# Optimization experiments

Hardware: AMD Instinct MI355X
Metric: run time of the kernel (lower is better)

Reference implementation:

```python
import jax, jax.numpy as jnp
import numpy as np

EPS = 1e-8  # torch F.cosine_similarity default eps


def setup_inputs() -> dict:
    key = jax.random.key(0)
    k1, k2 = jax.random.split(key)
    B, D, C = 8192, 1024, 1000
    x = jax.random.normal(k1, (B, D), dtype=jnp.float32)
    W = jax.random.normal(k2, (D, C), dtype=jnp.float32) * 0.02
    b = jnp.zeros((C,), dtype=jnp.float32)
    return {"x": x, "W": W, "b": b}


def reference(x, W, b):
    B = x.shape[0]
    # classifier logits -> softmax probs
    logits = x @ W + b                              # [B, C]
    logp = jax.nn.log_softmax(logits, axis=1)       # [B, C]
    pred = jnp.exp(logp)
    # per-row sum of p * log p (negative entropy), matches pred*log(pred) loop
    loss = jnp.sum(pred * logp, axis=-1)            # [B]
    # per-row mean cosine similarity against all rows (incl. self)
    norms = jnp.maximum(jnp.linalg.norm(x, axis=1, keepdims=True), EPS)
    xn = x / norms                                  # [B, D]
    sim = xn @ xn.T                                 # [B, B]
    weight = jnp.sum(sim, axis=1) / B               # [B]
    return loss * weight
```

## Files before the change

kernel.cpp:

```cpp
#include <hip/hip_runtime.h>
#include <hip/hip_bf16.h>
#include <cstdint>
#include <cstddef>

typedef __attribute__((ext_vector_type(8))) short bf16x8;
typedef __attribute__((ext_vector_type(4))) float f32x4;

__device__ __forceinline__ unsigned short f2bf(float f) {
  union { float f; unsigned u; } v; v.f = f;
  unsigned r = v.u + 0x7FFFu + ((v.u >> 16) & 1u);
  return (unsigned short)(r >> 16);
}

__device__ __forceinline__ float bf2f(unsigned short h) {
  union { float f; unsigned u; } c; c.u = ((unsigned)h) << 16;
  return c.f;
}

__device__ __forceinline__ void gload_lds16(const void* g, void* l) {
  __builtin_amdgcn_global_load_lds(
      (const __attribute__((address_space(1))) unsigned int*)g,
      (__attribute__((address_space(3))) unsigned int*)l, 16, 0, 0);
}

__global__ __launch_bounds__(1024) void k01_prep(const float* __restrict__ W,
                                                 unsigned short* __restrict__ Wt,
                                                 const float* __restrict__ x,
                                                 unsigned short* __restrict__ xbf,
                                                 float* __restrict__ rnorm,
                                                 float* __restrict__ s) {
  __shared__ __align__(16) char sm[82176];
  int tid = threadIdx.x;
  int b = blockIdx.x;
  int lane = tid & 63;
  int wid = tid >> 6;

  int k0 = (b & 15) * 64;
  int c0 = (b >> 4) * 64;
  int tx = tid & 63;
  int ty = tid >> 6;
  float wreg[4];
#pragma unroll
  for (int i = 0; i < 4; ++i) {
    int c = c0 + tx;
    wreg[i] = (c < 1000) ? W[(size_t)(k0 + i * 16 + ty) * 1000 + c] : 0.f;
  }

  {
    float (*sblk)[1024] = (float(*)[1024])sm;
    int row0 = b * 32 + wid * 2;
    const float4* xr0 = (const float4*)(x + (size_t)row0 * 1024);
    const float4* xr1 = (const float4*)(x + (size_t)(row0 + 1) * 1024);
    float4 v[2][4];
#pragma unroll
    for (int j = 0; j < 4; ++j) v[0][j] = xr0[lane + j * 64];
#pragma unroll
    for (int j = 0; j < 4; ++j) v[1][j] = xr1[lane + j * 64];
    float ss0 = 0.f, ss1 = 0.f;
#pragma unroll
    for (int j = 0; j < 4; ++j) {
      ss0 += v[0][j].x * v[0][j].x + v[0][j].y * v[0][j].y +
             v[0][j].z * v[0][j].z + v[0][j].w * v[0][j].w;
      ss1 += v[1][j].x * v[1][j].x + v[1][j].y * v[1][j].y +
             v[1][j].z * v[1][j].z + v[1][j].w * v[1][j].w;
    }
#pragma unroll
    for (int m = 1; m < 64; m <<= 1) {
      ss0 += __shfl_xor(ss0, m);
      ss1 += __shfl_xor(ss1, m);
    }
    float rn0 = 1.f / fmaxf(sqrtf(ss0), 1e-8f);
    float rn1 = 1.f / fmaxf(sqrtf(ss1), 1e-8f);
    if (lane == 0) {
      rnorm[row0] = rn0;
      rnorm[row0 + 1] = rn1;
    }
    float4 sacc[4];
#pragma unroll
    for (int j = 0; j < 4; ++j) {
      ushort4 h0, h1;
      h0.x = f2bf(v[0][j].x); h0.y = f2bf(v[0][j].y);
      h0.z = f2bf(v[0][j].z); h0.w = f2bf(v[0][j].w);
      h1.x = f2bf(v[1][j].x); h1.y = f2bf(v[1][j].y);
      h1.z = f2bf(v[1][j].z); h1.w = f2bf(v[1][j].w);
      ((ushort4*)(xbf + (size_t)row0 * 1024))[lane + j * 64] = h0;
      ((ushort4*)(xbf + (size_t)(row0 + 1) * 1024))[lane + j * 64] = h1;
      sacc[j].x = v[0][j].x * rn0 + v[1][j].x * rn1;
      sacc[j].y = v[0][j].y * rn0 + v[1][j].y * rn1;
      sacc[j].z = v[0][j].z * rn0 + v[1][j].z * rn1;
      sacc[j].w = v[0][j].w * rn0 + v[1][j].w * rn1;
    }
#pragma unroll
    for (int j = 0; j < 4; ++j) ((float4*)sblk[wid])[j * 64 + lane] = sacc[j];
    __syncthreads();
    float t = 0.f;
#pragma unroll
    for (int w = 0; w < 16; ++w) t += sblk[w][tid];
    atomicAdd(&s[tid], t);
  }

  {
    float (*tile)[65] = (float(*)[65])(sm + 65536);
#pragma unroll
    for (int i = 0; i < 4; ++i) tile[i * 16 + ty][tx] = wreg[i];
    __syncthreads();
#pragma unroll
    for (int i = 0; i < 4; ++i) {
      int ct = i * 16 + ty;
      Wt[(size_t)(c0 + ct) * 1024 + (k0 + tx)] = f2bf(tile[tx][ct]);
    }
  }
}

#define LDSBUF 49152

__global__ __launch_bounds__(512) void k3_gemm(const unsigned short* __restrict__ xbf,
                                               const unsigned short* __restrict__ wt,
                                               const float* __restrict__ bias,
                                               float* __restrict__ pm,
                                               float* __restrict__ pz,
                                               float* __restrict__ ps) {
  __shared__ __align__(16) char lds[147456];

  int tid = threadIdx.x;
  int lane = tid & 63;
  int wid = tid >> 6;
  int wc = wid & 1;
  int wr = wid >> 1;
  int cb = blockIdx.x >> 5;
  int rb = blockIdx.x & 31;
  int C0 = cb * 128;
  int R0 = rb * 256;

  float bv[4][4];
#pragma unroll
  for (int mf = 0; mf < 4; ++mf)
#pragma unroll
    for (int q = 0; q < 4; ++q) {
      int cls_g = C0 + wc * 64 + mf * 16 + (lane >> 4) * 4 + q;
      bv[mf][q] = (cls_g < 1000) ? bias[cls_g] : -1e30f;
    }
  f32x4 acc[4][4];
#pragma unroll
  for (int mf = 0; mf < 4; ++mf)
#pragma unroll
    for (int nf = 0; nf < 4; ++nf)
#pragma unroll
      for (int q = 0; q < 4; ++q) acc[mf][nf][q] = bv[mf][q];

  const char* gA = (const char*)(wt + (size_t)C0 * 1024);
  const char* gB = (const char*)(xbf + (size_t)R0 * 1024);
  int grow = lane >> 3;
  int gswz = ((lane & 7) ^ grow) << 4;

#define STA(kt, b, r)                                                          \
  gload_lds16(gA + (size_t)((r) * 64 + wid * 8 + grow) * 2048 + (kt) * 128 +   \
                  gswz,                                                        \
              lds + (b) * LDSBUF + (r) * 8192 + wid * 1024)
#define STB(kt, b, r)                                                          \
  gload_lds16(gB + (size_t)((r) * 64 + wid * 8 + grow) * 2048 + (kt) * 128 +   \
                  gswz,                                                        \
              lds + (b) * LDSBUF + 16384 + (r) * 8192 + wid * 1024)

  STA(0, 0, 0); STA(0, 0, 1); STB(0, 0, 0); STB(0, 0, 1); STB(0, 0, 2); STB(0, 0, 3);
  STA(1, 1, 0); STA(1, 1, 1); STB(1, 1, 0); STB(1, 1, 1); STB(1, 1, 2); STB(1, 1, 3);

  int rsw = (lane & 7) << 4;
  int kcol = (lane >> 4) * 16;

  auto ktile = [&](const char* A, const char* B, int nt, int nb, bool pf) {
    bf16x8 a[4][2];
#pragma unroll
    for (int mf = 0; mf < 4; ++mf)
#pragma unroll
      for (int ks = 0; ks < 2; ++ks)
        a[mf][ks] = *(const bf16x8*)(A + (wc * 64 + mf * 16 + (lane & 15)) * 128 +
                                     ((ks * 64 + kcol) ^ rsw));
    {
      bf16x8 b0[2];
#pragma unroll
      for (int ks = 0; ks < 2; ++ks)
        b0[ks] = *(const bf16x8*)(B + (wr * 64 + 0 * 16 + (lane & 15)) * 128 +
                                  ((ks * 64 + kcol) ^ rsw));
      if (pf) { STA(nt, nb, 0); STA(nt, nb, 1); }
      __builtin_amdgcn_s_barrier();
      __builtin_amdgcn_s_setprio(1);
#pragma unroll
      for (int ks = 0; ks < 2; ++ks)
#pragma unroll
        for (int mf = 0; mf < 4; ++mf)
          acc[mf][0] = __builtin_amdgcn_mfma_f32_16x16x32_bf16(a[mf][ks], b0[ks],
                                                               acc[mf][0], 0, 0, 0);
      __builtin_amdgcn_s_setprio(0);
      __builtin_amdgcn_s_barrier();
    }
    {
      bf16x8 b1[2];
#pragma unroll
      for (int ks = 0; ks < 2; ++ks)
        b1[ks] = *(const bf16x8*)(B + (wr * 64 + 1 * 16 + (lane & 15)) * 128 +
                                  ((ks * 64 + kcol) ^ rsw));
      if (pf) { STB(nt, nb, 0); STB(nt, nb, 1); }
      __builtin_amdgcn_s_barrier();
      __builtin_amdgcn_s_setprio(1);
#pragma unroll
      for (int ks = 0; ks < 2; ++ks)
#pragma unroll
        for (int mf = 0; mf < 4; ++mf)
          acc[mf][1] = __builtin_amdgcn_mfma_f32_16x16x32_bf16(a[mf][ks], b1[ks],
                                                               acc[mf][1], 0, 0, 0);
      __builtin_amdgcn_s_setprio(0);
      __builtin_amdgcn_s_barrier();
    }
    {
      bf16x8 b2[2];
#pragma unroll
      for (int ks = 0; ks < 2; ++ks)
        b2[ks] = *(const bf16x8*)(B + (wr * 64 + 2 * 16 + (lane & 15)) * 128 +
                                  ((ks * 64 + kcol) ^ rsw));
      if (pf) { STB(nt, nb, 2); STB(nt, nb, 3); }
      __builtin_amdgcn_s_barrier();
      __builtin_amdgcn_s_setprio(1);
#pragma unroll
      for (int ks = 0; ks < 2; ++ks)
#pragma unroll
        for (int mf = 0; mf < 4; ++mf)
          acc[mf][2] = __builtin_amdgcn_mfma_f32_16x16x32_bf16(a[mf][ks], b2[ks],
                                                               acc[mf][2], 0, 0, 0);
      __builtin_amdgcn_s_setprio(0);
      __builtin_amdgcn_s_barrier();
    }
    {
      bf16x8 b3[2];
#pragma unroll
      for (int ks = 0; ks < 2; ++ks)
        b3[ks] = *(const bf16x8*)(B + (wr * 64 + 3 * 16 + (lane & 15)) * 128 +
                                  ((ks * 64 + kcol) ^ rsw));
      __builtin_amdgcn_s_barrier();
      __builtin_amdgcn_s_setprio(1);
#pragma unroll
      for (int ks = 0; ks < 2; ++ks)
#pragma unroll
        for (int mf = 0; mf < 4; ++mf)
          acc[mf][3] = __builtin_amdgcn_mfma_f32_16x16x32_bf16(a[mf][ks], b3[ks],
                                                               acc[mf][3], 0, 0, 0);
      __builtin_amdgcn_s_setprio(0);
    }
  };

  for (int t = 0; t < 15; ++t) {
    asm volatile("s_waitcnt vmcnt(6)" ::: "memory");
    __builtin_amdgcn_s_barrier();
    asm volatile("" ::: "memory");
    const char* A = lds + (t % 3) * LDSBUF;
    ktile(A, A + 16384, t + 2, (t + 2) % 3, t < 14);
  }
  asm volatile("s_waitcnt vmcnt(0)" ::: "memory");
  __builtin_amdgcn_s_barrier();
  asm volatile("" ::: "memory");
  {
    const char* A = lds + (15 % 3) * LDSBUF;
    ktile(A, A + 16384, 0, 0, false);
  }

  __syncthreads();
  float* mm = (float*)lds;
  float* zz = mm + 512;
  float* sv = zz + 512;
#pragma unroll
  for (int nf = 0; nf < 4; ++nf) {
    float m1 = -1e30f;
#pragma unroll
    for (int mf = 0; mf < 4; ++mf)
#pragma unroll
      for (int q = 0; q < 4; ++q) m1 = fmaxf(m1, acc[mf][nf][q]);
    m1 = fmaxf(m1, __shfl_xor(m1, 16));
    m1 = fmaxf(m1, __shfl_xor(m1, 32));
    float z1 = 0.f, s1 = 0.f;
#pragma unroll
    for (int mf = 0; mf < 4; ++mf)
#pragma unroll
      for (int q = 0; q < 4; ++q) {
        float tt = acc[mf][nf][q] - m1;
        float e = expf(tt);
        z1 += e;
        s1 += e * tt;
      }
    z1 += __shfl_xor(z1, 16); z1 += __shfl_xor(z1, 32);
    s1 += __shfl_xor(s1, 16); s1 += __shfl_xor(s1, 32);
    if (lane < 16) {
      int r = wr * 64 + nf * 16 + lane;
      mm[wc * 256 + r] = m1;
      zz[wc * 256 + r] = z1;
      sv[wc * 256 + r] = s1;
    }
  }
  __syncthreads();
  if (tid < 256) {
    float m0 = mm[tid], mA = mm[256 + tid];
    float z0 = zz[tid], zA = zz[256 + tid];
    float s0 = sv[tid], sA = sv[256 + tid];
    float M = fmaxf(m0, mA);
    float e0 = expf(m0 - M), e1 = expf(mA - M);
    float Z = z0 * e0 + zA * e1;
    float S = e0 * (s0 + (m0 - M) * z0) + e1 * (sA + (mA - M) * zA);
    size_t o = (size_t)cb * 8192 + R0 + tid;
    pm[o] = M;
    pz[o] = Z;
    ps[o] = S;
  }
}

__global__ __launch_bounds__(256) void k4_final(const unsigned short* __restrict__ xbf,
                                                const float* __restrict__ s,
                                                const float* __restrict__ rnorm,
                                                const float* __restrict__ pm,
                                                const float* __restrict__ pz,
                                                const float* __restrict__ ps,
                                                float* __restrict__ out) {
  int tid = threadIdx.x;
  int wid = tid >> 6, lane = tid & 63;
  int row = blockIdx.x * 4 + wid;
  const bf16x8* xr = (const bf16x8*)(xbf + (size_t)row * 1024);
  const float4* s4 = (const float4*)s;
  float dot = 0.f;
#pragma unroll
  for (int j = 0; j < 2; ++j) {
    bf16x8 v = xr[lane + j * 64];
    float4 sa = s4[(lane + j * 64) * 2];
    float4 sb = s4[(lane + j * 64) * 2 + 1];
    dot += bf2f((unsigned short)v[0]) * sa.x + bf2f((unsigned short)v[1]) * sa.y +
           bf2f((unsigned short)v[2]) * sa.z + bf2f((unsigned short)v[3]) * sa.w +
           bf2f((unsigned short)v[4]) * sb.x + bf2f((unsigned short)v[5]) * sb.y +
           bf2f((unsigned short)v[6]) * sb.z + bf2f((unsigned short)v[7]) * sb.w;
  }
#pragma unroll
  for (int m = 1; m < 64; m <<= 1) dot += __shfl_xor(dot, m);
  if (lane == 0) {
    float mv[8], zv[8], svv[8];
    float M = -1e30f;
#pragma unroll
    for (int c = 0; c < 8; ++c) {
      mv[c] = pm[(size_t)c * 8192 + row];
      zv[c] = pz[(size_t)c * 8192 + row];
      svv[c] = ps[(size_t)c * 8192 + row];
      M = fmaxf(M, mv[c]);
    }
    float Z = 0.f, S = 0.f;
#pragma unroll
    for (int c = 0; c < 8; ++c) {
      float e = expf(mv[c] - M);
      Z += zv[c] * e;
      S += e * (svv[c] + (mv[c] - M) * zv[c]);
    }
    float loss = S / Z - logf(Z);
    out[row] = loss * dot * rnorm[row] * (1.f / 8192.f);
  }
}

extern "C" void kernel_launch(void* const* d_in, const int* in_sizes, int n_in,
                              void* d_out, int out_size, void* d_ws, size_t ws_size,
                              hipStream_t stream) {
  (void)in_sizes; (void)n_in; (void)out_size; (void)ws_size;
  const float* x = (const float*)d_in[0];
  const float* W = (const float*)d_in[1];
  const float* b = (const float*)d_in[2];
  float* out = (float*)d_out;
  char* ws = (char*)d_ws;

  unsigned short* Wt = (unsigned short*)(ws + 0);
  unsigned short* xbf = (unsigned short*)(ws + 2097152);
  float* rnorm = (float*)(ws + 18874368);
  float* s = (float*)(ws + 18907136);
  float* pm = (float*)(ws + 18915328);
  float* pz = (float*)(ws + 18915328 + 262144);
  float* ps = (float*)(ws + 18915328 + 524288);

  hipMemsetAsync(s, 0, 4096, stream);
  k01_prep<<<256, 1024, 0, stream>>>(W, Wt, x, xbf, rnorm, s);
  k3_gemm<<<256, 512, 0, stream>>>(xbf, Wt, b, pm, pz, ps);
  k4_final<<<2048, 256, 0, stream>>>(xbf, s, rnorm, pm, pz, ps, out);
}
```

Measured before the change: 52.22 us.

## Replace atomic column-sum with partial buffer reduction and simplify GEMM tiling

The prep kernel now writes per-block partial column sums to a buffer, and a new small reduction kernel sums them, replacing the memset plus atomicAdd path. The GEMM kernel moves from 512-thread blocks with 256-row tiles and a 3-stage, finely barriered pipeline to 256-thread blocks with 128-row tiles, a simple double buffer and one sync per k-step, launching twice as many blocks with less LDS each. This aims to remove atomic contention and raise occupancy, at the cost of an extra kernel launch and less overlap between loads and MFMA. The sp buffer aliases pm, which is safe only because the reduction kernel finishes before the GEMM writes pm.

```diff
diff --git a/kernel.cpp b/kernel.cpp
--- a/kernel.cpp
+++ b/kernel.cpp
@@ -28,7 +28,7 @@
                                                  const float* __restrict__ x,
                                                  unsigned short* __restrict__ xbf,
                                                  float* __restrict__ rnorm,
-                                                 float* __restrict__ s) {
+                                                 float* __restrict__ sp) {
   __shared__ __align__(16) char sm[82176];
   int tid = threadIdx.x;
   int b = blockIdx.x;
@@ -93,10 +93,10 @@
 #pragma unroll
     for (int j = 0; j < 4; ++j) ((float4*)sblk[wid])[j * 64 + lane] = sacc[j];
     __syncthreads();
-    float t = 0.f;
-#pragma unroll
-    for (int w = 0; w < 16; ++w) t += sblk[w][tid];
-    atomicAdd(&s[tid], t);
+    float acc = 0.f;
+#pragma unroll
+    for (int w = 0; w < 16; ++w) acc += sblk[w][tid];
+    sp[(size_t)b * 1024 + tid] = acc;
   }
 
   {
@@ -112,25 +112,38 @@
   }
 }
 
-#define LDSBUF 49152
-
-__global__ __launch_bounds__(512) void k3_gemm(const unsigned short* __restrict__ xbf,
+__global__ __launch_bounds__(256) void k2_sred(const float* __restrict__ sp,
+                                               float* __restrict__ s) {
+  __shared__ float red[4][64];
+  int t = threadIdx.x;
+  int dd = t & 63;
+  int g = t >> 6;
+  int d = blockIdx.x * 64 + dd;
+  float acc = 0.f;
+#pragma unroll 8
+  for (int b = g * 64; b < g * 64 + 64; ++b) acc += sp[(size_t)b * 1024 + d];
+  red[g][dd] = acc;
+  __syncthreads();
+  if (g == 0) s[d] = red[0][dd] + red[1][dd] + red[2][dd] + red[3][dd];
+}
+
+__global__ __launch_bounds__(256) void k3_gemm(const unsigned short* __restrict__ xbf,
                                                const unsigned short* __restrict__ wt,
                                                const float* __restrict__ bias,
                                                float* __restrict__ pm,
                                                float* __restrict__ pz,
                                                float* __restrict__ ps) {
-  __shared__ __align__(16) char lds[147456];
+  __shared__ __align__(16) char lds[65536];
 
   int tid = threadIdx.x;
   int lane = tid & 63;
   int wid = tid >> 6;
   int wc = wid & 1;
   int wr = wid >> 1;
-  int cb = blockIdx.x >> 5;
-  int rb = blockIdx.x & 31;
+  int cb = blockIdx.x >> 6;
+  int rb = blockIdx.x & 63;
   int C0 = cb * 128;
-  int R0 = rb * 256;
+  int R0 = rb * 128;
 
   float bv[4][4];
 #pragma unroll
@@ -150,123 +163,64 @@
 
   const char* gA = (const char*)(wt + (size_t)C0 * 1024);
   const char* gB = (const char*)(xbf + (size_t)R0 * 1024);
-  int grow = lane >> 3;
-  int gswz = ((lane & 7) ^ grow) << 4;
-
-#define STA(kt, b, r)                                                          \
-  gload_lds16(gA + (size_t)((r) * 64 + wid * 8 + grow) * 2048 + (kt) * 128 +   \
-                  gswz,                                                        \
-              lds + (b) * LDSBUF + (r) * 8192 + wid * 1024)
-#define STB(kt, b, r)                                                          \
-  gload_lds16(gB + (size_t)((r) * 64 + wid * 8 + grow) * 2048 + (kt) * 128 +   \
-                  gswz,                                                        \
-              lds + (b) * LDSBUF + 16384 + (r) * 8192 + wid * 1024)
-
-  STA(0, 0, 0); STA(0, 0, 1); STB(0, 0, 0); STB(0, 0, 1); STB(0, 0, 2); STB(0, 0, 3);
-  STA(1, 1, 0); STA(1, 1, 1); STB(1, 1, 0); STB(1, 1, 1); STB(1, 1, 2); STB(1, 1, 3);
+  int grow = (tid >> 3) & 7;
+  int gswz = ((tid & 7) ^ grow) << 4;
+
+  auto stage = [&](int kt, int bb) {
+    char* lA = lds + bb * 32768;
+    char* lB = lA + 16384;
+#pragma unroll
+    for (int i = 0; i < 4; ++i) {
+      size_t row = i * 32 + (tid >> 3);
+      gload_lds16(gA + row * 2048 + kt * 128 + gswz, lA + i * 4096 + tid * 16);
+    }
+#pragma unroll
+    for (int i = 0; i < 4; ++i) {
+      size_t row = i * 32 + (tid >> 3);
+      gload_lds16(gB + row * 2048 + kt * 128 + gswz, lB + i * 4096 + tid * 16);
+    }
+  };
 
   int rsw = (lane & 7) << 4;
   int kcol = (lane >> 4) * 16;
 
-  auto ktile = [&](const char* A, const char* B, int nt, int nb, bool pf) {
-    bf16x8 a[4][2];
+  stage(0, 0);
+  __syncthreads();
+  int cur = 0;
+  for (int t = 0; t < 16; ++t) {
+    if (t < 15) stage(t + 1, cur ^ 1);
+    const char* A = lds + cur * 32768;
+    const char* B = A + 16384;
+    bf16x8 a[4][2], bb[4][2];
 #pragma unroll
     for (int mf = 0; mf < 4; ++mf)
 #pragma unroll
       for (int ks = 0; ks < 2; ++ks)
         a[mf][ks] = *(const bf16x8*)(A + (wc * 64 + mf * 16 + (lane & 15)) * 128 +
                                      ((ks * 64 + kcol) ^ rsw));
-    {
-      bf16x8 b0[2];
+#pragma unroll
+    for (int nf = 0; nf < 4; ++nf)
 #pragma unroll
       for (int ks = 0; ks < 2; ++ks)
-        b0[ks] = *(const bf16x8*)(B + (wr * 64 + 0 * 16 + (lane & 15)) * 128 +
-                                  ((ks * 64 + kcol) ^ rsw));
-      if (pf) { STA(nt, nb, 0); STA(nt, nb, 1); }
-      __builtin_amdgcn_s_barrier();
-      __builtin_amdgcn_s_setprio(1);
-#pragma unroll
-      for (int ks = 0; ks < 2; ++ks)
-#pragma unroll
-        for (int mf = 0; mf < 4; ++mf)
-          acc[mf][0] = __builtin_amdgcn_mfma_f32_16x16x32_bf16(a[mf][ks], b0[ks],
-                                                               acc[mf][0], 0, 0, 0);
-      __builtin_amdgcn_s_setprio(0);
-      __builtin_amdgcn_s_barrier();
-    }
-    {
-      bf16x8 b1[2];
-#pragma unroll
-      for (int ks = 0; ks < 2; ++ks)
-        b1[ks] = *(const bf16x8*)(B + (wr * 64 + 1 * 16 + (lane & 15)) * 128 +
-                                  ((ks * 64 + kcol) ^ rsw));
-      if (pf) { STB(nt, nb, 0); STB(nt, nb, 1); }
-      __builtin_amdgcn_s_barrier();
-      __builtin_amdgcn_s_setprio(1);
-#pragma unroll
-      for (int ks = 0; ks < 2; ++ks)
-#pragma unroll
-        for (int mf = 0; mf < 4; ++mf)
-          acc[mf][1] = __builtin_amdgcn_mfma_f32_16x16x32_bf16(a[mf][ks], b1[ks],
-                                                               acc[mf][1], 0, 0, 0);
-      __builtin_amdgcn_s_setprio(0);
-      __builtin_amdgcn_s_barrier();
-    }
-    {
-      bf16x8 b2[2];
-#pragma unroll
-      for (int ks = 0; ks < 2; ++ks)
-        b2[ks] = *(const bf16x8*)(B + (wr * 64 + 2 * 16 + (lane & 15)) * 128 +
-                                  ((ks * 64 + kcol) ^ rsw));
-      if (pf) { STB(nt, nb, 2); STB(nt, nb, 3); }
-      __builtin_amdgcn_s_barrier();
-      __builtin_amdgcn_s_setprio(1);
-#pragma unroll
-      for (int ks = 0; ks < 2; ++ks)
-#pragma unroll
-        for (int mf = 0; mf < 4; ++mf)
-          acc[mf][2] = __builtin_amdgcn_mfma_f32_16x16x32_bf16(a[mf][ks], b2[ks],
-                                                               acc[mf][2], 0, 0, 0);
-      __builtin_amdgcn_s_setprio(0);
-      __builtin_amdgcn_s_barrier();
-    }
-    {
-      bf16x8 b3[2];
-#pragma unroll
-      for (int ks = 0; ks < 2; ++ks)
-        b3[ks] = *(const bf16x8*)(B + (wr * 64 + 3 * 16 + (lane & 15)) * 128 +
-                                  ((ks * 64 + kcol) ^ rsw));
-      __builtin_amdgcn_s_barrier();
-      __builtin_amdgcn_s_setprio(1);
-#pragma unroll
-      for (int ks = 0; ks < 2; ++ks)
-#pragma unroll
-        for (int mf = 0; mf < 4; ++mf)
-          acc[mf][3] = __builtin_amdgcn_mfma_f32_16x16x32_bf16(a[mf][ks], b3[ks],
-                                                               acc[mf][3], 0, 0, 0);
-      __builtin_amdgcn_s_setprio(0);
-    }
-  };
-
-  for (int t = 0; t < 15; ++t) {
-    asm volatile("s_waitcnt vmcnt(6)" ::: "memory");
-    __builtin_amdgcn_s_barrier();
-    asm volatile("" ::: "memory");
-    const char* A = lds + (t % 3) * LDSBUF;
-    ktile(A, A + 16384, t + 2, (t + 2) % 3, t < 14);
-  }
-  asm volatile("s_waitcnt vmcnt(0)" ::: "memory");
-  __builtin_amdgcn_s_barrier();
-  asm volatile("" ::: "memory");
-  {
-    const char* A = lds + (15 % 3) * LDSBUF;
-    ktile(A, A + 16384, 0, 0, false);
-  }
-
-  __syncthreads();
+        bb[nf][ks] = *(const bf16x8*)(B + (wr * 64 + nf * 16 + (lane & 15)) * 128 +
+                                      ((ks * 64 + kcol) ^ rsw));
+    __builtin_amdgcn_s_setprio(1);
+#pragma unroll
+    for (int ks = 0; ks < 2; ++ks)
+#pragma unroll
+      for (int mf = 0; mf < 4; ++mf)
+#pragma unroll
+        for (int nf = 0; nf < 4; ++nf)
+          acc[mf][nf] = __builtin_amdgcn_mfma_f32_16x16x32_bf16(a[mf][ks], bb[nf][ks],
+                                                                acc[mf][nf], 0, 0, 0);
+    __builtin_amdgcn_s_setprio(0);
+    __syncthreads();
+    cur ^= 1;
+  }
+
   float* mm = (float*)lds;
-  float* zz = mm + 512;
-  float* sv = zz + 512;
+  float* zz = mm + 256;
+  float* sv = zz + 256;
 #pragma unroll
   for (int nf = 0; nf < 4; ++nf) {
     float m1 = -1e30f;
@@ -290,16 +244,16 @@
     s1 += __shfl_xor(s1, 16); s1 += __shfl_xor(s1, 32);
     if (lane < 16) {
       int r = wr * 64 + nf * 16 + lane;
-      mm[wc * 256 + r] = m1;
-      zz[wc * 256 + r] = z1;
-      sv[wc * 256 + r] = s1;
+      mm[wc * 128 + r] = m1;
+      zz[wc * 128 + r] = z1;
+      sv[wc * 128 + r] = s1;
     }
   }
   __syncthreads();
-  if (tid < 256) {
-    float m0 = mm[tid], mA = mm[256 + tid];
-    float z0 = zz[tid], zA = zz[256 + tid];
-    float s0 = sv[tid], sA = sv[256 + tid];
+  if (tid < 128) {
+    float m0 = mm[tid], mA = mm[128 + tid];
+    float z0 = zz[tid], zA = zz[128 + tid];
+    float s0 = sv[tid], sA = sv[128 + tid];
     float M = fmaxf(m0, mA);
     float e0 = expf(m0 - M), e1 = expf(mA - M);
     float Z = z0 * e0 + zA * e1;
@@ -372,12 +326,13 @@
   unsigned short* xbf = (unsigned short*)(ws + 2097152);
   float* rnorm = (float*)(ws + 18874368);
   float* s = (float*)(ws + 18907136);
+  float* sp = (float*)(ws + 18915328);
   float* pm = (float*)(ws + 18915328);
   float* pz = (float*)(ws + 18915328 + 262144);
   float* ps = (float*)(ws + 18915328 + 524288);
 
-  hipMemsetAsync(s, 0, 4096, stream);
-  k01_prep<<<256, 1024, 0, stream>>>(W, Wt, x, xbf, rnorm, s);
-  k3_gemm<<<256, 512, 0, stream>>>(xbf, Wt, b, pm, pz, ps);
+  k01_prep<<<256, 1024, 0, stream>>>(W, Wt, x, xbf, rnorm, sp);
+  k2_sred<<<16, 256, 0, stream>>>(sp, s);
+  k3_gemm<<<512, 256, 0, stream>>>(xbf, Wt, b, pm, pz, ps);
   k4_final<<<2048, 256, 0, stream>>>(xbf, s, rnorm, pm, pz, ps, out);
 }
```

Measured after the change: 52.58 us. Within noise of the previous version (+0.7%).
